# Kernel optimization log

Hardware: AMD Instinct MI355X
Metric: run time of the kernel (lower is better)

The kernel has to match this reference:

```python
import jax, jax.numpy as jnp
import numpy as np

B = 16384          # batch size
NUM_NEG = 4
N = 1 + NUM_NEG    # items per row (pos + negs)
D = 128            # embedding_dim
F = 4              # num_factors
FS = D // F        # factor_size = 32
TD = 384           # bert_text_dim
NU = 100000        # num_users
NI = 100000        # num_items
HID = 150          # text MLP hidden
M = 2              # num_modalities


def _linear_init(k, fan_out, fan_in):
    bound = 1.0 / np.sqrt(fan_in)
    return jax.random.uniform(k, (fan_out, fan_in), jnp.float32, -bound, bound)


def setup_inputs() -> dict:
    key = jax.random.key(0)
    ks = jax.random.split(key, 12)
    batch = jax.random.randint(ks[0], (B, 1 + N), 0, NU)          # col0=user, cols1..5=items
    text = jax.random.normal(ks[1], (B, N, TD), dtype=jnp.float32)
    user_table = jax.random.normal(ks[2], (NU, D), dtype=jnp.float32)
    item_table = jax.random.normal(ks[3], (NI, D), dtype=jnp.float32)
    w1 = _linear_init(ks[4], HID, TD)
    b1 = jax.random.uniform(ks[5], (HID,), jnp.float32, -1/np.sqrt(TD), 1/np.sqrt(TD))
    w2 = _linear_init(ks[6], D, HID)
    b2 = jax.random.uniform(ks[7], (D,), jnp.float32, -1/np.sqrt(HID), 1/np.sqrt(HID))
    # per-factor attention MLPs, stacked over the F factors (all same size here)
    aw1 = jax.random.uniform(ks[8], (F, M, 3 * FS), jnp.float32, -1/np.sqrt(3*FS), 1/np.sqrt(3*FS))
    ab1 = jax.random.uniform(ks[9], (F, M), jnp.float32, -1/np.sqrt(3*FS), 1/np.sqrt(3*FS))
    aw2 = jax.random.uniform(ks[10], (F, M, M), jnp.float32, -1/np.sqrt(M), 1/np.sqrt(M))
    return dict(batch=batch, text=text, user_table=user_table, item_table=item_table,
                w1=w1, b1=b1, w2=w2, b2=b2, aw1=aw1, ab1=ab1, aw2=aw2)


def _leaky_relu(x):
    return jnp.where(x > 0, x, 0.01 * x)


def reference(batch, text, user_table, item_table, w1, b1, w2, b2, aw1, ab1, aw2):
    # text MLP: Linear -> LeakyReLU -> Linear -> LeakyReLU
    te = _leaky_relu(_leaky_relu(text @ w1.T + b1) @ w2.T + b2)   # [B,N,D]

    users = batch[:, 0]
    items = batch[:, 1:]
    u = user_table[users]                                          # [B,D]
    ie = item_table[items]                                         # [B,N,D]

    # split into F factors of size FS (vectorized over factor dim)
    uf = jnp.broadcast_to(u[:, None, :], ie.shape).reshape(B, N, F, FS)
    itf = ie.reshape(B, N, F, FS)
    tf = te.reshape(B, N, F, FS)

    cat = jnp.concatenate([uf, itf, tf], axis=-1)                  # [B,N,F,3*FS]
    nrm = jnp.linalg.norm(cat, axis=-1, keepdims=True)
    cat = cat / jnp.maximum(nrm, 1e-12)                            # F.normalize(dim=-1)

    h = jnp.tanh(jnp.einsum('bnfk,fmk->bnfm', cat, aw1) + ab1)     # [B,N,F,M]
    logits = jnp.einsum('bnfm,fom->bnfo', h, aw2)                  # [B,N,F,M]
    # torch nn.Softmax() with dim=None on a 3D tensor -> softmax over dim 0 (batch)
    attn = jax.nn.softmax(logits, axis=0)

    r_ui = attn[..., 0] * jax.nn.softplus(jnp.sum(uf * itf, axis=-1))  # [B,N,F]
    r_ut = attn[..., 1] * jax.nn.softplus(jnp.sum(uf * tf, axis=-1))   # [B,N,F]
    ratings = jnp.sum(r_ui + r_ut, axis=-1)                        # [B,N], sum over factors
    return ratings
```

## Files before the change

### kernel.cpp

```cpp
#include <hip/hip_runtime.h>
#include <hip/hip_bf16.h>

#define TDIM 384
#define HID 150
#define DD 128
#define ROWS 81920
#define RT 32

typedef __attribute__((ext_vector_type(8))) short short8;
typedef __attribute__((ext_vector_type(4))) float f32x4;

#define SMEM_BYTES 16896

__device__ __forceinline__ float lrelu(float x) { return x > 0.f ? x : 0.01f * x; }
__device__ __forceinline__ float softplusf(float x) {
    return fmaxf(x, 0.f) + log1pf(expf(-fabsf(x)));
}

__device__ __forceinline__ short8 pack8(const float4 a, const float4 b) {
    union { short8 s; __hip_bfloat16 h[8]; } u;
    u.h[0] = __float2bfloat16(a.x); u.h[1] = __float2bfloat16(a.y);
    u.h[2] = __float2bfloat16(a.z); u.h[3] = __float2bfloat16(a.w);
    u.h[4] = __float2bfloat16(b.x); u.h[5] = __float2bfloat16(b.y);
    u.h[6] = __float2bfloat16(b.z); u.h[7] = __float2bfloat16(b.w);
    return u.s;
}

__global__ __launch_bounds__(256)
void prep_w(const float* __restrict__ w1, const float* __restrict__ w2,
            short8* __restrict__ w1fT, short8* __restrict__ w2fT)
{
    const int idx = blockIdx.x * 256 + threadIdx.x;
    union { short8 s; __hip_bfloat16 h[8]; } u;
    if (idx < 7680) {
        const int kt  = idx / 640;
        const int rem = idx % 640;
        const int g   = rem / 320;
        const int r2  = rem % 320;
        const int tj  = r2 / 64;
        const int ln  = r2 % 64;
        const int quad = ln >> 4, m16 = ln & 15;
        const int col = g * 80 + tj * 16 + m16;
        const int k   = kt * 32 + quad * 8;
#pragma unroll
        for (int j = 0; j < 8; ++j)
            u.h[j] = __float2bfloat16(col < HID ? w1[(size_t)col * TDIM + k + j] : 0.f);
        w1fT[idx] = u.s;
    } else if (idx < 10240) {
        const int i2  = idx - 7680;
        const int kt  = i2 / 512;
        const int rem = i2 % 512;
        const int g   = rem / 256;
        const int r2  = rem % 256;
        const int tj  = r2 / 64;
        const int ln  = r2 % 64;
        const int quad = ln >> 4, m16 = ln & 15;
        const int col = g * 64 + tj * 16 + m16;
        const int k   = kt * 32 + quad * 8;
#pragma unroll
        for (int j = 0; j < 8; ++j)
            u.h[j] = __float2bfloat16((k + j) < HID ? w2[(size_t)col * HID + k + j] : 0.f);
        w2fT[i2] = u.s;
    }
}

__global__ __launch_bounds__(256, 8)
void fused_main(const int* __restrict__ batch,
                const float* __restrict__ text,
                const float* __restrict__ user_table,
                const float* __restrict__ item_table,
                const short8* __restrict__ w1fT,
                const float* __restrict__ b1,
                const short8* __restrict__ w2fT,
                const float* __restrict__ b2,
                const float* __restrict__ aw1,
                const float* __restrict__ ab1,
                const float* __restrict__ aw2,
                float* __restrict__ expp,
                float* __restrict__ Sglob)
{
    __shared__ __align__(16) unsigned char smem[SMEM_BYTES];
    __shared__ __align__(8) float red[RT * 8];
    __hip_bfloat16* Hs = (__hip_bfloat16*)(smem);
    float*          Ts = (float*)(smem);

    const int t    = threadIdx.x;
    const int r0   = blockIdx.x * RT;
    const int lane = t & 63;
    const int wv   = t >> 6;
    const int m16  = lane & 15;
    const int quad = lane >> 4;
    const int g    = wv >> 1;
    const int wr   = (wv & 1) * 16;
    const int wc   = g * 80;
    const int wc2  = g * 64;

    const int p3row = t >> 3;
    const int p3f   = (t >> 1) & 3;
    const int half  = t & 1;
    const int gr    = r0 + p3row;
    const int bb    = gr / 5;
    const int nn    = gr - bb * 5;

    const float* ta  = text + (size_t)(r0 + wr + m16) * TDIM;
    const int    ko0 = quad * 8;
    const int w1base = g * 320 + lane;

    f32x4 acc1[5];
#pragma unroll
    for (int j = 0; j < 5; ++j) acc1[j] = (f32x4){0.f, 0.f, 0.f, 0.f};

    float4 pA[2][2];
#pragma unroll
    for (int k = 0; k < 2; ++k) {
        pA[k][0] = *(const float4*)(ta + k * 32 + ko0);
        pA[k][1] = *(const float4*)(ta + k * 32 + ko0 + 4);
    }

#pragma unroll
    for (int kt = 0; kt < 12; ++kt) {
        const int p = kt & 1;
        short8 bw[5];
#pragma unroll
        for (int tj = 0; tj < 5; ++tj)
            bw[tj] = w1fT[kt * 640 + w1base + tj * 64];
        const short8 a0 = pack8(pA[p][0], pA[p][1]);
        if (kt < 10) {
            const int ko = (kt + 2) * 32 + ko0;
            pA[p][0] = *(const float4*)(ta + ko);
            pA[p][1] = *(const float4*)(ta + ko + 4);
        }
#pragma unroll
        for (int tj = 0; tj < 5; ++tj)
            acc1[tj] = __builtin_amdgcn_mfma_f32_16x16x32_bf16(a0, bw[tj], acc1[tj], 0, 0, 0);
    }

#pragma unroll
    for (int tj = 0; tj < 5; ++tj) {
        const int col = wc + tj * 16 + m16;
        const float bv = (col < HID) ? b1[col] : 0.f;
#pragma unroll
        for (int r = 0; r < 4; ++r) {
            const int row = wr + quad * 4 + r;
            float v = lrelu(acc1[tj][r] + bv);
            if (col >= HID) v = 0.f;
            Hs[row * 168 + col] = __float2bfloat16(v);
        }
    }
    __syncthreads();

    f32x4 acc2[4];
#pragma unroll
    for (int j = 0; j < 4; ++j) acc2[j] = (f32x4){0.f, 0.f, 0.f, 0.f};

    const __hip_bfloat16* h0p = Hs + (wr + m16) * 168 + ko0;
    const int w2base = g * 256 + lane;

#pragma unroll
    for (int kt = 0; kt < 5; ++kt) {
        short8 bw[4];
#pragma unroll
        for (int tj = 0; tj < 4; ++tj)
            bw[tj] = w2fT[kt * 512 + w2base + tj * 64];
        const short8 a0 = *(const short8*)(h0p + kt * 32);
#pragma unroll
        for (int tj = 0; tj < 4; ++tj)
            acc2[tj] = __builtin_amdgcn_mfma_f32_16x16x32_bf16(a0, bw[tj], acc2[tj], 0, 0, 0);
    }
    __syncthreads();

#pragma unroll
    for (int tj = 0; tj < 4; ++tj) {
        const int col = wc2 + tj * 16 + m16;
        const float bv = b2[col];
#pragma unroll
        for (int r = 0; r < 4; ++r) {
            const int row = wr + quad * 4 + r;
            Ts[row * 132 + col] = lrelu(acc2[tj][r] + bv);
        }
    }

    const int uid = batch[bb * 6];
    const int iid = batch[bb * 6 + 1 + nn];
    const float* up = user_table + (size_t)uid * DD + p3f * 32 + half * 16;
    const float* ip = item_table + (size_t)iid * DD + p3f * 32 + half * 16;
    float4 ur[4], er[4];
#pragma unroll
    for (int q = 0; q < 4; ++q) {
        ur[q] = *(const float4*)(up + q * 4);
        er[q] = *(const float4*)(ip + q * 4);
    }
    __syncthreads();

    {
        const float* tp  = Ts + p3row * 132 + p3f * 32 + half * 16;
        const float* a1p = aw1 + p3f * 192 + half * 16;

        float ss = 0.f, z0 = 0.f, z1 = 0.f, sui = 0.f, sut = 0.f;
#pragma unroll
        for (int q = 0; q < 4; ++q) {
            const float4 u4 = ur[q];
            const float4 e4 = er[q];
            const float4 t4 = *(const float4*)(tp + q * 4);
            const float4 a00 = *(const float4*)(a1p + q * 4);
            const float4 a01 = *(const float4*)(a1p + 32 + q * 4);
            const float4 a02 = *(const float4*)(a1p + 64 + q * 4);
            const float4 a10 = *(const float4*)(a1p + 96 + q * 4);
            const float4 a11 = *(const float4*)(a1p + 128 + q * 4);
            const float4 a12 = *(const float4*)(a1p + 160 + q * 4);
            const float uu[4] = {u4.x, u4.y, u4.z, u4.w};
            const float ee[4] = {e4.x, e4.y, e4.z, e4.w};
            const float tt[4] = {t4.x, t4.y, t4.z, t4.w};
            const float w00[4] = {a00.x, a00.y, a00.z, a00.w};
            const float w01[4] = {a01.x, a01.y, a01.z, a01.w};
            const float w02[4] = {a02.x, a02.y, a02.z, a02.w};
            const float w10[4] = {a10.x, a10.y, a10.z, a10.w};
            const float w11[4] = {a11.x, a11.y, a11.z, a11.w};
            const float w12[4] = {a12.x, a12.y, a12.z, a12.w};
#pragma unroll
            for (int c = 0; c < 4; ++c) {
                const float u = uu[c], e = ee[c], x = tt[c];
                ss  = fmaf(u, u, ss); ss = fmaf(e, e, ss); ss = fmaf(x, x, ss);
                z0  = fmaf(u, w00[c], z0);
                z0  = fmaf(e, w01[c], z0);
                z0  = fmaf(x, w02[c], z0);
                z1  = fmaf(u, w10[c], z1);
                z1  = fmaf(e, w11[c], z1);
                z1  = fmaf(x, w12[c], z1);
                sui = fmaf(u, e, sui);
                sut = fmaf(u, x, sut);
            }
        }
        ss  += __shfl_xor(ss, 1);
        z0  += __shfl_xor(z0, 1);
        z1  += __shfl_xor(z1, 1);
        sui += __shfl_xor(sui, 1);
        sut += __shfl_xor(sut, 1);

        const float inv = 1.f / fmaxf(sqrtf(ss), 1e-12f);
        const float h0 = tanhf(fmaf(z0, inv, ab1[p3f * 2 + 0]));
        const float h1 = tanhf(fmaf(z1, inv, ab1[p3f * 2 + 1]));
        const float l0 = fmaf(h0, aw2[p3f * 4 + 0], h1 * aw2[p3f * 4 + 1]);
        const float l1 = fmaf(h0, aw2[p3f * 4 + 2], h1 * aw2[p3f * 4 + 3]);
        const float e0 = expf(l0), e1 = expf(l1);
        const float pui = softplusf(sui), put = softplusf(sut);
        if (half == 0) {
            *(float4*)&expp[((size_t)gr * 4 + p3f) * 4] = make_float4(e0, e1, pui, put);
            *(float2*)&red[p3row * 8 + p3f * 2] = make_float2(e0, e1);
        }
    }
    __syncthreads();

    if (t < 40) {
        const int j   = t & 7;
        const int nn0 = t >> 3;
        const int rep = blockIdx.x & 7;
        int r = nn0 - (r0 % 5);
        if (r < 0) r += 5;
        float s = 0.f;
        for (; r < RT; r += 5) s += red[r * 8 + j];
        atomicAdd(&Sglob[((t * 8) + rep) * 16], s);
    }
}

__global__ __launch_bounds__(256)
void finalize(const float* __restrict__ expp,
              const float* __restrict__ Sglob,
              float* __restrict__ out)
{
    __shared__ float Ss[40];
    const int t = threadIdx.x;

    if (t < 160) {
        const int cidx = t >> 2;
        const int rp   = t & 3;
        float v = Sglob[(cidx * 8 + rp * 2 + 0) * 16]
                + Sglob[(cidx * 8 + rp * 2 + 1) * 16];
        v += __shfl_xor(v, 1);
        v += __shfl_xor(v, 2);
        if (rp == 0) Ss[cidx] = v;
    }
    __syncthreads();

    const int gr = blockIdx.x * 256 + t;
    const int b = gr / 5;
    const int n = gr - b * 5;
    float r = 0.f;
#pragma unroll
    for (int f = 0; f < 4; ++f) {
        const float4 v = *(const float4*)&expp[((size_t)gr * 4 + f) * 4];
        const float S0 = Ss[n * 8 + f * 2 + 0];
        const float S1 = Ss[n * 8 + f * 2 + 1];
        r += v.x / S0 * v.z + v.y / S1 * v.w;
    }
    out[gr] = r;
}

extern "C" void kernel_launch(void* const* d_in, const int* in_sizes, int n_in,
                              void* d_out, int out_size, void* d_ws, size_t ws_size,
                              hipStream_t stream)
{
    (void)in_sizes; (void)n_in; (void)out_size; (void)ws_size;
    const int*   batch      = (const int*)d_in[0];
    const float* text       = (const float*)d_in[1];
    const float* user_table = (const float*)d_in[2];
    const float* item_table = (const float*)d_in[3];
    const float* w1         = (const float*)d_in[4];
    const float* b1         = (const float*)d_in[5];
    const float* w2         = (const float*)d_in[6];
    const float* b2         = (const float*)d_in[7];
    const float* aw1        = (const float*)d_in[8];
    const float* ab1        = (const float*)d_in[9];
    const float* aw2        = (const float*)d_in[10];
    float* out = (float*)d_out;

    char* ws = (char*)d_ws;
    short8* w1fT  = (short8*)ws;
    short8* w2fT  = (short8*)(ws + 122880);
    float*  expp  = (float*)(ws + 163840);
    float*  Sglob = (float*)(ws + 163840 + (size_t)ROWS * 16 * 4);

    hipMemsetAsync(Sglob, 0, 320 * 16 * sizeof(float), stream);
    prep_w<<<40, 256, 0, stream>>>(w1, w2, w1fT, w2fT);
    fused_main<<<ROWS / RT, 256, 0, stream>>>(batch, text, user_table, item_table,
                                              w1fT, b1, w2fT, b2, aw1, ab1, aw2,
                                              expp, Sglob);
    finalize<<<ROWS / 256, 256, 0, stream>>>(expp, Sglob, out);
}
```

Measured before the change: 327.6 us.

## Restructure fused kernel to single-wave blocks of 16 rows without barriers

The fused kernel now runs one 64-lane wave per block covering 16 rows. That wave computes all 160 hidden columns and 128 output columns itself, so every __syncthreads is removed and the shuffle reductions disappear because each lane handles a whole factor. Weight prepacking is reindexed to match the new column order, and the softmax-denominator atomics are spread over 32 replicas to reduce contention. In exchange, each wave holds more accumulator registers and each block reloads the full weight set from L2 for only 16 rows, which cuts weight reuse per load.

```diff
diff --git a/kernel.cpp b/kernel.cpp
--- a/kernel.cpp
+++ b/kernel.cpp
@@ -5,12 +5,13 @@
 #define HID 150
 #define DD 128
 #define ROWS 81920
-#define RT 32
+#define RT 16
+#define NREP 32
 
 typedef __attribute__((ext_vector_type(8))) short short8;
 typedef __attribute__((ext_vector_type(4))) float f32x4;
 
-#define SMEM_BYTES 16896
+#define SMEM_BYTES 8448
 
 __device__ __forceinline__ float lrelu(float x) { return x > 0.f ? x : 0.01f * x; }
 __device__ __forceinline__ float softplusf(float x) {
@@ -35,12 +36,10 @@
     if (idx < 7680) {
         const int kt  = idx / 640;
         const int rem = idx % 640;
-        const int g   = rem / 320;
-        const int r2  = rem % 320;
-        const int tj  = r2 / 64;
-        const int ln  = r2 % 64;
+        const int jj  = rem / 64;
+        const int ln  = rem % 64;
         const int quad = ln >> 4, m16 = ln & 15;
-        const int col = g * 80 + tj * 16 + m16;
+        const int col = jj * 16 + m16;
         const int k   = kt * 32 + quad * 8;
 #pragma unroll
         for (int j = 0; j < 8; ++j)
@@ -50,12 +49,10 @@
         const int i2  = idx - 7680;
         const int kt  = i2 / 512;
         const int rem = i2 % 512;
-        const int g   = rem / 256;
-        const int r2  = rem % 256;
-        const int tj  = r2 / 64;
-        const int ln  = r2 % 64;
+        const int jj  = rem / 64;
+        const int ln  = rem % 64;
         const int quad = ln >> 4, m16 = ln & 15;
-        const int col = g * 64 + tj * 16 + m16;
+        const int col = jj * 16 + m16;
         const int k   = kt * 32 + quad * 8;
 #pragma unroll
         for (int j = 0; j < 8; ++j)
@@ -64,7 +61,7 @@
     }
 }
 
-__global__ __launch_bounds__(256, 8)
+__global__ __launch_bounds__(64, 4)
 void fused_main(const int* __restrict__ batch,
                 const float* __restrict__ text,
                 const float* __restrict__ user_table,
@@ -84,31 +81,26 @@
     __hip_bfloat16* Hs = (__hip_bfloat16*)(smem);
     float*          Ts = (float*)(smem);
 
-    const int t    = threadIdx.x;
+    const int lane = threadIdx.x;
     const int r0   = blockIdx.x * RT;
-    const int lane = t & 63;
-    const int wv   = t >> 6;
     const int m16  = lane & 15;
     const int quad = lane >> 4;
-    const int g    = wv >> 1;
-    const int wr   = (wv & 1) * 16;
-    const int wc   = g * 80;
-    const int wc2  = g * 64;
-
-    const int p3row = t >> 3;
-    const int p3f   = (t >> 1) & 3;
-    const int half  = t & 1;
+    const int ko0  = quad * 8;
+
+    const int p3row = lane >> 2;
+    const int p3f   = lane & 3;
     const int gr    = r0 + p3row;
     const int bb    = gr / 5;
     const int nn    = gr - bb * 5;
 
-    const float* ta  = text + (size_t)(r0 + wr + m16) * TDIM;
-    const int    ko0 = quad * 8;
-    const int w1base = g * 320 + lane;
-
-    f32x4 acc1[5];
-#pragma unroll
-    for (int j = 0; j < 5; ++j) acc1[j] = (f32x4){0.f, 0.f, 0.f, 0.f};
+    const int uid = batch[bb * 6];
+    const int iid = batch[bb * 6 + 1 + nn];
+
+    const float* ta = text + (size_t)(r0 + m16) * TDIM;
+
+    f32x4 acc1[10];
+#pragma unroll
+    for (int j = 0; j < 10; ++j) acc1[j] = (f32x4){0.f, 0.f, 0.f, 0.f};
 
     float4 pA[2][2];
 #pragma unroll
@@ -120,10 +112,10 @@
 #pragma unroll
     for (int kt = 0; kt < 12; ++kt) {
         const int p = kt & 1;
-        short8 bw[5];
-#pragma unroll
-        for (int tj = 0; tj < 5; ++tj)
-            bw[tj] = w1fT[kt * 640 + w1base + tj * 64];
+        short8 bw[10];
+#pragma unroll
+        for (int jj = 0; jj < 10; ++jj)
+            bw[jj] = w1fT[kt * 640 + jj * 64 + lane];
         const short8 a0 = pack8(pA[p][0], pA[p][1]);
         if (kt < 10) {
             const int ko = (kt + 2) * 32 + ko0;
@@ -131,74 +123,68 @@
             pA[p][1] = *(const float4*)(ta + ko + 4);
         }
 #pragma unroll
-        for (int tj = 0; tj < 5; ++tj)
-            acc1[tj] = __builtin_amdgcn_mfma_f32_16x16x32_bf16(a0, bw[tj], acc1[tj], 0, 0, 0);
-    }
-
-#pragma unroll
-    for (int tj = 0; tj < 5; ++tj) {
-        const int col = wc + tj * 16 + m16;
+        for (int jj = 0; jj < 10; ++jj)
+            acc1[jj] = __builtin_amdgcn_mfma_f32_16x16x32_bf16(a0, bw[jj], acc1[jj], 0, 0, 0);
+    }
+
+#pragma unroll
+    for (int jj = 0; jj < 10; ++jj) {
+        const int col = jj * 16 + m16;
         const float bv = (col < HID) ? b1[col] : 0.f;
 #pragma unroll
         for (int r = 0; r < 4; ++r) {
-            const int row = wr + quad * 4 + r;
-            float v = lrelu(acc1[tj][r] + bv);
+            const int row = quad * 4 + r;
+            float v = lrelu(acc1[jj][r] + bv);
             if (col >= HID) v = 0.f;
             Hs[row * 168 + col] = __float2bfloat16(v);
         }
     }
-    __syncthreads();
-
-    f32x4 acc2[4];
-#pragma unroll
-    for (int j = 0; j < 4; ++j) acc2[j] = (f32x4){0.f, 0.f, 0.f, 0.f};
-
-    const __hip_bfloat16* h0p = Hs + (wr + m16) * 168 + ko0;
-    const int w2base = g * 256 + lane;
+
+    f32x4 acc2[8];
+#pragma unroll
+    for (int j = 0; j < 8; ++j) acc2[j] = (f32x4){0.f, 0.f, 0.f, 0.f};
+
+    const __hip_bfloat16* h0p = Hs + m16 * 168 + ko0;
 
 #pragma unroll
     for (int kt = 0; kt < 5; ++kt) {
-        short8 bw[4];
-#pragma unroll
-        for (int tj = 0; tj < 4; ++tj)
-            bw[tj] = w2fT[kt * 512 + w2base + tj * 64];
+        short8 cw[8];
+#pragma unroll
+        for (int jj = 0; jj < 8; ++jj)
+            cw[jj] = w2fT[kt * 512 + jj * 64 + lane];
         const short8 a0 = *(const short8*)(h0p + kt * 32);
 #pragma unroll
-        for (int tj = 0; tj < 4; ++tj)
-            acc2[tj] = __builtin_amdgcn_mfma_f32_16x16x32_bf16(a0, bw[tj], acc2[tj], 0, 0, 0);
-    }
-    __syncthreads();
-
-#pragma unroll
-    for (int tj = 0; tj < 4; ++tj) {
-        const int col = wc2 + tj * 16 + m16;
-        const float bv = b2[col];
-#pragma unroll
-        for (int r = 0; r < 4; ++r) {
-            const int row = wr + quad * 4 + r;
-            Ts[row * 132 + col] = lrelu(acc2[tj][r] + bv);
-        }
-    }
-
-    const int uid = batch[bb * 6];
-    const int iid = batch[bb * 6 + 1 + nn];
-    const float* up = user_table + (size_t)uid * DD + p3f * 32 + half * 16;
-    const float* ip = item_table + (size_t)iid * DD + p3f * 32 + half * 16;
-    float4 ur[4], er[4];
-#pragma unroll
-    for (int q = 0; q < 4; ++q) {
+        for (int jj = 0; jj < 8; ++jj)
+            acc2[jj] = __builtin_amdgcn_mfma_f32_16x16x32_bf16(a0, cw[jj], acc2[jj], 0, 0, 0);
+    }
+
+    const float* up = user_table + (size_t)uid * DD + p3f * 32;
+    const float* ip = item_table + (size_t)iid * DD + p3f * 32;
+    float4 ur[8], er[8];
+#pragma unroll
+    for (int q = 0; q < 8; ++q) {
         ur[q] = *(const float4*)(up + q * 4);
         er[q] = *(const float4*)(ip + q * 4);
     }
-    __syncthreads();
+
+#pragma unroll
+    for (int jj = 0; jj < 8; ++jj) {
+        const int col = jj * 16 + m16;
+        const float bv = b2[col];
+#pragma unroll
+        for (int r = 0; r < 4; ++r) {
+            const int row = quad * 4 + r;
+            Ts[row * 132 + col] = lrelu(acc2[jj][r] + bv);
+        }
+    }
 
     {
-        const float* tp  = Ts + p3row * 132 + p3f * 32 + half * 16;
-        const float* a1p = aw1 + p3f * 192 + half * 16;
+        const float* tp  = Ts + p3row * 132 + p3f * 32;
+        const float* a1p = aw1 + p3f * 192;
 
         float ss = 0.f, z0 = 0.f, z1 = 0.f, sui = 0.f, sut = 0.f;
 #pragma unroll
-        for (int q = 0; q < 4; ++q) {
+        for (int q = 0; q < 8; ++q) {
             const float4 u4 = ur[q];
             const float4 e4 = er[q];
             const float4 t4 = *(const float4*)(tp + q * 4);
@@ -231,12 +217,6 @@
                 sut = fmaf(u, x, sut);
             }
         }
-        ss  += __shfl_xor(ss, 1);
-        z0  += __shfl_xor(z0, 1);
-        z1  += __shfl_xor(z1, 1);
-        sui += __shfl_xor(sui, 1);
-        sut += __shfl_xor(sut, 1);
-
         const float inv = 1.f / fmaxf(sqrtf(ss), 1e-12f);
         const float h0 = tanhf(fmaf(z0, inv, ab1[p3f * 2 + 0]));
         const float h1 = tanhf(fmaf(z1, inv, ab1[p3f * 2 + 1]));
@@ -244,22 +224,19 @@
         const float l1 = fmaf(h0, aw2[p3f * 4 + 2], h1 * aw2[p3f * 4 + 3]);
         const float e0 = expf(l0), e1 = expf(l1);
         const float pui = softplusf(sui), put = softplusf(sut);
-        if (half == 0) {
-            *(float4*)&expp[((size_t)gr * 4 + p3f) * 4] = make_float4(e0, e1, pui, put);
-            *(float2*)&red[p3row * 8 + p3f * 2] = make_float2(e0, e1);
-        }
-    }
-    __syncthreads();
-
-    if (t < 40) {
-        const int j   = t & 7;
-        const int nn0 = t >> 3;
-        const int rep = blockIdx.x & 7;
+        *(float4*)&expp[((size_t)gr * 4 + p3f) * 4] = make_float4(e0, e1, pui, put);
+        *(float2*)&red[p3row * 8 + p3f * 2] = make_float2(e0, e1);
+    }
+
+    if (lane < 40) {
+        const int j   = lane & 7;
+        const int nn0 = lane >> 3;
+        const int rep = blockIdx.x & (NREP - 1);
         int r = nn0 - (r0 % 5);
         if (r < 0) r += 5;
         float s = 0.f;
         for (; r < RT; r += 5) s += red[r * 8 + j];
-        atomicAdd(&Sglob[((t * 8) + rep) * 16], s);
+        atomicAdd(&Sglob[((size_t)rep * 40 + lane) * 16], s);
     }
 }
 
@@ -271,14 +248,12 @@
     __shared__ float Ss[40];
     const int t = threadIdx.x;
 
-    if (t < 160) {
-        const int cidx = t >> 2;
-        const int rp   = t & 3;
-        float v = Sglob[(cidx * 8 + rp * 2 + 0) * 16]
-                + Sglob[(cidx * 8 + rp * 2 + 1) * 16];
-        v += __shfl_xor(v, 1);
-        v += __shfl_xor(v, 2);
-        if (rp == 0) Ss[cidx] = v;
+    if (t < 40) {
+        float s = 0.f;
+#pragma unroll
+        for (int rep = 0; rep < NREP; ++rep)
+            s += Sglob[((size_t)rep * 40 + t) * 16];
+        Ss[t] = s;
     }
     __syncthreads();
 
@@ -320,10 +295,10 @@
     float*  expp  = (float*)(ws + 163840);
     float*  Sglob = (float*)(ws + 163840 + (size_t)ROWS * 16 * 4);
 
-    hipMemsetAsync(Sglob, 0, 320 * 16 * sizeof(float), stream);
+    hipMemsetAsync(Sglob, 0, (size_t)NREP * 40 * 16 * sizeof(float), stream);
     prep_w<<<40, 256, 0, stream>>>(w1, w2, w1fT, w2fT);
-    fused_main<<<ROWS / RT, 256, 0, stream>>>(batch, text, user_table, item_table,
-                                              w1fT, b1, w2fT, b2, aw1, ab1, aw2,
-                                              expp, Sglob);
+    fused_main<<<ROWS / RT, 64, 0, stream>>>(batch, text, user_table, item_table,
+                                             w1fT, b1, w2fT, b2, aw1, ab1, aw2,
+                                             expp, Sglob);
     finalize<<<ROWS / 256, 256, 0, stream>>>(expp, Sglob, out);
 }
```

New measurement: 361.7 us. +10.4%, slower.

## Stage text tile through LDS as bf16 with coalesced loads before MFMA

Applied to the files above, without the earlier changes.

The text tile is now loaded once by the whole block with fully coalesced float4 reads, converted to bf16 and stored in padded LDS. MFMA A-fragments are then read from LDS instead of being loaded per lane as scattered strided global rows. This removes uncoalesced global access, but the old register prefetch that overlapped loads with MFMA is gone, and extra barriers are added. Occupancy drops from 8 to 6 blocks because the larger LDS footprint now also holds the reduction buffer.

```diff
diff --git a/kernel.cpp b/kernel.cpp
--- a/kernel.cpp
+++ b/kernel.cpp
@@ -10,20 +10,12 @@
 typedef __attribute__((ext_vector_type(8))) short short8;
 typedef __attribute__((ext_vector_type(4))) float f32x4;
 
-#define SMEM_BYTES 16896
+#define SMEM_BYTES 25088
+#define TASTRIDE 392
 
 __device__ __forceinline__ float lrelu(float x) { return x > 0.f ? x : 0.01f * x; }
 __device__ __forceinline__ float softplusf(float x) {
     return fmaxf(x, 0.f) + log1pf(expf(-fabsf(x)));
-}
-
-__device__ __forceinline__ short8 pack8(const float4 a, const float4 b) {
-    union { short8 s; __hip_bfloat16 h[8]; } u;
-    u.h[0] = __float2bfloat16(a.x); u.h[1] = __float2bfloat16(a.y);
-    u.h[2] = __float2bfloat16(a.z); u.h[3] = __float2bfloat16(a.w);
-    u.h[4] = __float2bfloat16(b.x); u.h[5] = __float2bfloat16(b.y);
-    u.h[6] = __float2bfloat16(b.z); u.h[7] = __float2bfloat16(b.w);
-    return u.s;
 }
 
 __global__ __launch_bounds__(256)
@@ -64,7 +56,7 @@
     }
 }
 
-__global__ __launch_bounds__(256, 8)
+__global__ __launch_bounds__(256, 6)
 void fused_main(const int* __restrict__ batch,
                 const float* __restrict__ text,
                 const float* __restrict__ user_table,
@@ -80,9 +72,10 @@
                 float* __restrict__ Sglob)
 {
     __shared__ __align__(16) unsigned char smem[SMEM_BYTES];
-    __shared__ __align__(8) float red[RT * 8];
-    __hip_bfloat16* Hs = (__hip_bfloat16*)(smem);
-    float*          Ts = (float*)(smem);
+    __hip_bfloat16* tA  = (__hip_bfloat16*)(smem);
+    __hip_bfloat16* Hs  = (__hip_bfloat16*)(smem);
+    float*          Ts  = (float*)(smem);
+    float*          red = (float*)(smem + 16896);
 
     const int t    = threadIdx.x;
     const int r0   = blockIdx.x * RT;
@@ -102,38 +95,44 @@
     const int bb    = gr / 5;
     const int nn    = gr - bb * 5;
 
-    const float* ta  = text + (size_t)(r0 + wr + m16) * TDIM;
-    const int    ko0 = quad * 8;
+    {
+        const float* tbase = text + (size_t)r0 * TDIM;
+#pragma unroll
+        for (int i = 0; i < 12; ++i) {
+            const int fi  = i * 1024 + t * 4;
+            const int row = fi / TDIM;
+            const int k   = fi - row * TDIM;
+            const float4 v = *(const float4*)(tbase + fi);
+            union { __hip_bfloat16 h[4]; unsigned long long q; } o;
+            o.h[0] = __float2bfloat16(v.x);
+            o.h[1] = __float2bfloat16(v.y);
+            o.h[2] = __float2bfloat16(v.z);
+            o.h[3] = __float2bfloat16(v.w);
+            *(unsigned long long*)(tA + row * TASTRIDE + k) = o.q;
+        }
+    }
+    __syncthreads();
+
+    const int ko0 = quad * 8;
+    const __hip_bfloat16* tAp = tA + (wr + m16) * TASTRIDE + ko0;
     const int w1base = g * 320 + lane;
 
     f32x4 acc1[5];
 #pragma unroll
     for (int j = 0; j < 5; ++j) acc1[j] = (f32x4){0.f, 0.f, 0.f, 0.f};
 
-    float4 pA[2][2];
-#pragma unroll
-    for (int k = 0; k < 2; ++k) {
-        pA[k][0] = *(const float4*)(ta + k * 32 + ko0);
-        pA[k][1] = *(const float4*)(ta + k * 32 + ko0 + 4);
-    }
-
 #pragma unroll
     for (int kt = 0; kt < 12; ++kt) {
-        const int p = kt & 1;
         short8 bw[5];
 #pragma unroll
         for (int tj = 0; tj < 5; ++tj)
             bw[tj] = w1fT[kt * 640 + w1base + tj * 64];
-        const short8 a0 = pack8(pA[p][0], pA[p][1]);
-        if (kt < 10) {
-            const int ko = (kt + 2) * 32 + ko0;
-            pA[p][0] = *(const float4*)(ta + ko);
-            pA[p][1] = *(const float4*)(ta + ko + 4);
-        }
+        const short8 a0 = *(const short8*)(tAp + kt * 32);
 #pragma unroll
         for (int tj = 0; tj < 5; ++tj)
             acc1[tj] = __builtin_amdgcn_mfma_f32_16x16x32_bf16(a0, bw[tj], acc1[tj], 0, 0, 0);
     }
+    __syncthreads();
 
 #pragma unroll
     for (int tj = 0; tj < 5; ++tj) {
```

Result: faster. 300.9 us (-8.1%).
